# Kernel tuning notes

Measured on AMD Instinct MI355X. Metric: run time of the kernel, lower is better.

Reference implementation:

```python
import jax, jax.numpy as jnp
import numpy as np

TEMPERATURE = 0.07
NEG_INF_FILL = -1e9  # matches torch fill_diagonal_(-1000000000.0)


def setup_inputs() -> dict:
    key = jax.random.key(0)
    feats = jax.random.normal(key, (6144, 768), dtype=jnp.float32)
    return {"feats": feats}


def reference(feats):
    # L2-normalize rows (torch F.normalize uses eps=1e-12 clamp on the norm)
    norm = jnp.maximum(jnp.linalg.norm(feats, axis=1, keepdims=True), 1e-12)
    f = feats / norm
    N = f.shape[0]
    sim = jnp.matmul(f, f.T) / TEMPERATURE            # [N, N]
    eye = jnp.eye(N, dtype=bool)
    sim = jnp.where(eye, NEG_INF_FILL, sim)           # fill diagonal
    labels = jnp.arange(N) // 3                       # 3 views per slice
    pos = (labels[:, None] == labels[None, :]) & ~eye  # positives, self excluded
    # masked logsumexp over positives via weights b (grad-safe masking)
    numerator = jax.scipy.special.logsumexp(sim, axis=1, b=pos.astype(sim.dtype))
    denominator = jax.scipy.special.logsumexp(sim, axis=1)
    loss = jnp.sum(-(numerator - denominator)) / N
    return loss
```

## Files before the change

### kernel.cpp

```cpp
#include <hip/hip_runtime.h>

#define NN 6144
#define DD 768
#define NB 48
#define NTILES 1176
#define INV_T 14.285714285714286f
#define CMAX  14.285714285714286f

typedef int i32x4 __attribute__((ext_vector_type(4)));
typedef int i32x8 __attribute__((ext_vector_type(8)));
typedef float f32x4_t __attribute__((ext_vector_type(4)));

__device__ __forceinline__ void load_lds16(const void* g, void* l) {
    __builtin_amdgcn_global_load_lds((__attribute__((address_space(1))) void*)g,
                                     (__attribute__((address_space(3))) void*)l,
                                     16, 0, 0);
}

__global__ void norm_kernel(const float* __restrict__ feats,
                            unsigned int* __restrict__ fb8,
                            float* __restrict__ den_num) {
    const int wid = threadIdx.x >> 6;
    const int lane = threadIdx.x & 63;
    const int row = blockIdx.x * 4 + wid;

    if (threadIdx.x < 8) den_num[blockIdx.x * 8 + threadIdx.x] = 0.0f;

    const float4* src = (const float4*)(feats + (size_t)row * DD);
    float4 v[3];
    float ss = 0.0f;
#pragma unroll
    for (int i = 0; i < 3; ++i) {
        v[i] = src[lane + i * 64];
        ss += v[i].x * v[i].x + v[i].y * v[i].y + v[i].z * v[i].z + v[i].w * v[i].w;
    }
#pragma unroll
    for (int m = 32; m >= 1; m >>= 1) ss += __shfl_xor(ss, m);
    const float sc = 1.0f / fmaxf(sqrtf(ss), 1e-12f);

#pragma unroll
    for (int i = 0; i < 3; ++i) {
        unsigned int w = 0;
        w = __builtin_amdgcn_cvt_pk_fp8_f32(v[i].x * sc, v[i].y * sc, w, 0);
        w = __builtin_amdgcn_cvt_pk_fp8_f32(v[i].z * sc, v[i].w * sc, w, 1);
        fb8[(size_t)row * 192 + lane + i * 64] = w;
    }
}

__global__ __launch_bounds__(256, 2) void gemm_expsum_kernel(
        const unsigned char* __restrict__ fb8,
        float* __restrict__ den_sum, float* __restrict__ num_sum) {
    __shared__ __align__(16) char sA[128 * 128];
    __shared__ __align__(16) char sB[128 * 128];

    int rem = blockIdx.x;
    int bi = 0, rowlen = NB;
    while (rem >= rowlen) { rem -= rowlen; rowlen--; bi++; }
    const int bj = bi + rem;
    const bool isdiag = (bi == bj);
    const bool neardiag = (bj - bi) <= 1;
    const int i0 = bi * 128;
    const int j0 = bj * 128;

    const int t = threadIdx.x;
    const int lane = t & 63;
    const int wid = t >> 6;
    const int wm = wid >> 1;
    const int wn = wid & 1;

    const int srow = t >> 3;
    const int scb = ((t & 7) ^ (srow & 7)) * 16;
    const unsigned char* gA = fb8 + (size_t)(i0 + srow) * DD + scb;
    const unsigned char* gB = fb8 + (size_t)(j0 + srow) * DD + scb;
    char* ldsA = sA + wid * 1024;
    char* ldsB = sB + wid * 1024;

    f32x4_t acc[4][4];
    const f32x4_t zz = {0.0f, 0.0f, 0.0f, 0.0f};
#pragma unroll
    for (int mi = 0; mi < 4; ++mi)
#pragma unroll
        for (int ni = 0; ni < 4; ++ni) acc[mi][ni] = zz;

    const int q = lane >> 4;
    const int mrow = lane & 15;
    const int x7 = lane & 7;
    const int c0 = ((q << 1) ^ x7) << 4;
    const int c1 = (((q << 1) | 1) ^ x7) << 4;

#pragma unroll 1
    for (int kb = 0; kb < 6; ++kb) {
        const int k0 = kb * 128;
#pragma unroll
        for (int i = 0; i < 4; ++i) {
            load_lds16(gA + (size_t)(i * 32) * DD + k0, ldsA + i * 4096);
            load_lds16(gB + (size_t)(i * 32) * DD + k0, ldsB + i * 4096);
        }
        __syncthreads();

        i32x8 af[4];
#pragma unroll
        for (int mi = 0; mi < 4; ++mi) {
            const char* p = sA + (wm * 64 + mi * 16 + mrow) * 128;
            i32x4 lo = *(const i32x4*)(p + c0);
            i32x4 hi = *(const i32x4*)(p + c1);
            af[mi] = __builtin_shufflevector(lo, hi, 0, 1, 2, 3, 4, 5, 6, 7);
        }
#pragma unroll
        for (int ni = 0; ni < 4; ++ni) {
            const char* p = sB + (wn * 64 + ni * 16 + mrow) * 128;
            i32x4 lo = *(const i32x4*)(p + c0);
            i32x4 hi = *(const i32x4*)(p + c1);
            i32x8 bf = __builtin_shufflevector(lo, hi, 0, 1, 2, 3, 4, 5, 6, 7);
#pragma unroll
            for (int mi = 0; mi < 4; ++mi)
                acc[mi][ni] = __builtin_amdgcn_mfma_scale_f32_16x16x128_f8f6f4(
                    af[mi], bf, acc[mi][ni], 0, 0,
                    0, 0x7F7F7F7F, 0, 0x7F7F7F7F);
        }
        __syncthreads();
    }

    const int colb = j0 + wn * 64 + mrow;
    const int rowb = i0 + wm * 64 + (q << 2);
    float cs[4] = {0.f, 0.f, 0.f, 0.f};
    float csn[4] = {0.f, 0.f, 0.f, 0.f};
#pragma unroll
    for (int mi = 0; mi < 4; ++mi) {
        float rsv[4] = {0.f, 0.f, 0.f, 0.f};
        float rsn[4] = {0.f, 0.f, 0.f, 0.f};
#pragma unroll
        for (int ni = 0; ni < 4; ++ni) {
            const int col = colb + ni * 16;
#pragma unroll
            for (int r = 0; r < 4; ++r) {
                const int row = rowb + mi * 16 + r;
                const float v = acc[mi][ni][r] * INV_T;
                float e = __expf(v - CMAX);
                if (isdiag && row == col) e = 0.0f;
                rsv[r] += e;
                cs[ni] += e;
                if (neardiag && (row / 3 == col / 3) && row != col) {
                    rsn[r] += e;
                    csn[ni] += e;
                }
            }
        }
#pragma unroll
        for (int r = 0; r < 4; ++r) {
            float v = rsv[r];
            v += __shfl_xor(v, 8);
            v += __shfl_xor(v, 4);
            v += __shfl_xor(v, 2);
            v += __shfl_xor(v, 1);
            if (mrow == 0) atomicAdd(&den_sum[rowb + mi * 16 + r], v);
        }
        if (neardiag) {
#pragma unroll
            for (int r = 0; r < 4; ++r) {
                float v = rsn[r];
                v += __shfl_xor(v, 8);
                v += __shfl_xor(v, 4);
                v += __shfl_xor(v, 2);
                v += __shfl_xor(v, 1);
                if (mrow == 0) atomicAdd(&num_sum[rowb + mi * 16 + r], v);
            }
        }
    }
    if (!isdiag) {
#pragma unroll
        for (int ni = 0; ni < 4; ++ni) {
            float v = cs[ni];
            v += __shfl_xor(v, 16);
            v += __shfl_xor(v, 32);
            if (q == 0) atomicAdd(&den_sum[colb + ni * 16], v);
        }
        if (neardiag) {
#pragma unroll
            for (int ni = 0; ni < 4; ++ni) {
                float v = csn[ni];
                v += __shfl_xor(v, 16);
                v += __shfl_xor(v, 32);
                if (q == 0) atomicAdd(&num_sum[colb + ni * 16], v);
            }
        }
    }
}

__global__ void finalize_kernel(const float* __restrict__ den_sum,
                                const float* __restrict__ num_sum,
                                float* __restrict__ out) {
    float local = 0.0f;
    for (int i = threadIdx.x; i < NN; i += 256) {
        local += logf(den_sum[i]) - logf(num_sum[i]);
    }
#pragma unroll
    for (int m = 32; m >= 1; m >>= 1) local += __shfl_xor(local, m);
    __shared__ float ws[4];
    if ((threadIdx.x & 63) == 0) ws[threadIdx.x >> 6] = local;
    __syncthreads();
    if (threadIdx.x == 0) out[0] = (ws[0] + ws[1] + ws[2] + ws[3]) / (float)NN;
}

extern "C" void kernel_launch(void* const* d_in, const int* in_sizes, int n_in,
                              void* d_out, int out_size, void* d_ws, size_t ws_size,
                              hipStream_t stream) {
    const float* feats = (const float*)d_in[0];
    float* out = (float*)d_out;

    char* ws = (char*)d_ws;
    unsigned int* fb8 = (unsigned int*)ws;
    float* den_num    = (float*)(ws + 4718592);
    float* den_sum    = den_num;
    float* num_sum    = den_num + NN;

    norm_kernel<<<NN / 4, 256, 0, stream>>>(feats, fb8, den_num);
    gemm_expsum_kernel<<<NTILES, 256, 0, stream>>>((const unsigned char*)fb8,
                                                   den_sum, num_sum);
    finalize_kernel<<<1, 256, 0, stream>>>(den_sum, num_sum, out);
}
```

Before: 110.7 us.

## Double-buffer LDS tiles to overlap global loads with MFMA compute

Splits the A/B LDS tiles into two buffers each and fully unrolls the six K-steps so the next tile's global-to-LDS loads are issued before the current tile's MFMAs run. Only one barrier per step remains instead of two. It also folds the temperature scale and max shift into a single fma before exp. LDS use doubles to 64 KB per block, which may cut how many blocks fit per CU under the two-block launch bound.

New measurement: 195.4 us. +76.6%, slower.

```diff
diff --git a/kernel.cpp b/kernel.cpp
--- a/kernel.cpp
+++ b/kernel.cpp
@@ -50,8 +50,10 @@
 __global__ __launch_bounds__(256, 2) void gemm_expsum_kernel(
         const unsigned char* __restrict__ fb8,
         float* __restrict__ den_sum, float* __restrict__ num_sum) {
-    __shared__ __align__(16) char sA[128 * 128];
-    __shared__ __align__(16) char sB[128 * 128];
+    __shared__ __align__(16) char sA0[128 * 128];
+    __shared__ __align__(16) char sA1[128 * 128];
+    __shared__ __align__(16) char sB0[128 * 128];
+    __shared__ __align__(16) char sB1[128 * 128];
 
     int rem = blockIdx.x;
     int bi = 0, rowlen = NB;
@@ -72,8 +74,7 @@
     const int scb = ((t & 7) ^ (srow & 7)) * 16;
     const unsigned char* gA = fb8 + (size_t)(i0 + srow) * DD + scb;
     const unsigned char* gB = fb8 + (size_t)(j0 + srow) * DD + scb;
-    char* ldsA = sA + wid * 1024;
-    char* ldsB = sB + wid * 1024;
+    const int ldsoff = wid * 1024;
 
     f32x4_t acc[4][4];
     const f32x4_t zz = {0.0f, 0.0f, 0.0f, 0.0f};
@@ -88,38 +89,50 @@
     const int c0 = ((q << 1) ^ x7) << 4;
     const int c1 = (((q << 1) | 1) ^ x7) << 4;
 
-#pragma unroll 1
-    for (int kb = 0; kb < 6; ++kb) {
-        const int k0 = kb * 128;
-#pragma unroll
-        for (int i = 0; i < 4; ++i) {
-            load_lds16(gA + (size_t)(i * 32) * DD + k0, ldsA + i * 4096);
-            load_lds16(gB + (size_t)(i * 32) * DD + k0, ldsB + i * 4096);
-        }
-        __syncthreads();
-
-        i32x8 af[4];
-#pragma unroll
-        for (int mi = 0; mi < 4; ++mi) {
-            const char* p = sA + (wm * 64 + mi * 16 + mrow) * 128;
-            i32x4 lo = *(const i32x4*)(p + c0);
-            i32x4 hi = *(const i32x4*)(p + c1);
-            af[mi] = __builtin_shufflevector(lo, hi, 0, 1, 2, 3, 4, 5, 6, 7);
-        }
-#pragma unroll
-        for (int ni = 0; ni < 4; ++ni) {
-            const char* p = sB + (wn * 64 + ni * 16 + mrow) * 128;
-            i32x4 lo = *(const i32x4*)(p + c0);
-            i32x4 hi = *(const i32x4*)(p + c1);
-            i32x8 bf = __builtin_shufflevector(lo, hi, 0, 1, 2, 3, 4, 5, 6, 7);
-#pragma unroll
-            for (int mi = 0; mi < 4; ++mi)
-                acc[mi][ni] = __builtin_amdgcn_mfma_scale_f32_16x16x128_f8f6f4(
-                    af[mi], bf, acc[mi][ni], 0, 0,
-                    0, 0x7F7F7F7F, 0, 0x7F7F7F7F);
-        }
-        __syncthreads();
-    }
+#define STAGE(dstA, dstB, k0)                                                 \
+    {                                                                         \
+        _Pragma("unroll")                                                     \
+        for (int i = 0; i < 4; ++i) {                                         \
+            load_lds16(gA + (size_t)(i * 32) * DD + (k0), (dstA) + ldsoff + i * 4096); \
+            load_lds16(gB + (size_t)(i * 32) * DD + (k0), (dstB) + ldsoff + i * 4096); \
+        }                                                                     \
+    }
+
+#define COMPUTE(srcA, srcB)                                                   \
+    {                                                                         \
+        i32x8 af[4];                                                          \
+        _Pragma("unroll")                                                     \
+        for (int mi = 0; mi < 4; ++mi) {                                      \
+            const char* p = (srcA) + (wm * 64 + mi * 16 + mrow) * 128;        \
+            i32x4 lo = *(const i32x4*)(p + c0);                               \
+            i32x4 hi = *(const i32x4*)(p + c1);                               \
+            af[mi] = __builtin_shufflevector(lo, hi, 0, 1, 2, 3, 4, 5, 6, 7); \
+        }                                                                     \
+        _Pragma("unroll")                                                     \
+        for (int ni = 0; ni < 4; ++ni) {                                      \
+            const char* p = (srcB) + (wn * 64 + ni * 16 + mrow) * 128;        \
+            i32x4 lo = *(const i32x4*)(p + c0);                               \
+            i32x4 hi = *(const i32x4*)(p + c1);                               \
+            i32x8 bf = __builtin_shufflevector(lo, hi, 0, 1, 2, 3, 4, 5, 6, 7); \
+            _Pragma("unroll")                                                 \
+            for (int mi = 0; mi < 4; ++mi)                                    \
+                acc[mi][ni] = __builtin_amdgcn_mfma_scale_f32_16x16x128_f8f6f4( \
+                    af[mi], bf, acc[mi][ni], 0, 0,                            \
+                    0, 0x7F7F7F7F, 0, 0x7F7F7F7F);                            \
+        }                                                                     \
+    }
+
+    STAGE(sA0, sB0, 0);
+    __syncthreads();
+    STAGE(sA1, sB1, 128);  COMPUTE(sA0, sB0);  __syncthreads();
+    STAGE(sA0, sB0, 256);  COMPUTE(sA1, sB1);  __syncthreads();
+    STAGE(sA1, sB1, 384);  COMPUTE(sA0, sB0);  __syncthreads();
+    STAGE(sA0, sB0, 512);  COMPUTE(sA1, sB1);  __syncthreads();
+    STAGE(sA1, sB1, 640);  COMPUTE(sA0, sB0);  __syncthreads();
+    COMPUTE(sA1, sB1);
+
+#undef STAGE
+#undef COMPUTE
 
     const int colb = j0 + wn * 64 + mrow;
     const int rowb = i0 + wm * 64 + (q << 2);
@@ -135,8 +148,7 @@
 #pragma unroll
             for (int r = 0; r < 4; ++r) {
                 const int row = rowb + mi * 16 + r;
-                const float v = acc[mi][ni][r] * INV_T;
-                float e = __expf(v - CMAX);
+                float e = __expf(__builtin_fmaf(acc[mi][ni][r], INV_T, -CMAX));
                 if (isdiag && row == col) e = 0.0f;
                 rsv[r] += e;
                 cs[ni] += e;
```

## Switch to per-wave 64x64 tiles with direct global loads and 32x32 MFMA

Applied to the files above, without the earlier changes.

Replaces the 128x128 LDS-staged block tile with independent per-wave 64x64 upper-triangle tiles, loaded straight from global memory into registers with no LDS and no barriers. Tiles are grouped into 24x24 super-blocks and split into 8 chunks for locality, and the 16x16x128 MFMA is swapped for 32x32x64 MFMA. The goal is to remove LDS and sync overhead and raise occupancy, at the cost of less data reuse per wave (more global/L2 traffic) and more atomics per output row.

Measured after the change: 162.8 us. 1.47x slower.

```diff
diff --git a/kernel.cpp b/kernel.cpp
--- a/kernel.cpp
+++ b/kernel.cpp
@@ -2,19 +2,19 @@
 
 #define NN 6144
 #define DD 768
-#define NB 48
-#define NTILES 1176
 #define INV_T 14.285714285714286f
 #define CMAX  14.285714285714286f
 
+#define NWT 582
+
 typedef int i32x4 __attribute__((ext_vector_type(4)));
 typedef int i32x8 __attribute__((ext_vector_type(8)));
-typedef float f32x4_t __attribute__((ext_vector_type(4)));
-
-__device__ __forceinline__ void load_lds16(const void* g, void* l) {
-    __builtin_amdgcn_global_load_lds((__attribute__((address_space(1))) void*)g,
-                                     (__attribute__((address_space(3))) void*)l,
-                                     16, 0, 0);
+typedef float f32x16 __attribute__((ext_vector_type(16)));
+
+__device__ __forceinline__ i32x8 ld32B(const unsigned char* p) {
+    i32x4 lo = *(const i32x4*)p;
+    i32x4 hi = *(const i32x4*)(p + 16);
+    return __builtin_shufflevector(lo, hi, 0, 1, 2, 3, 4, 5, 6, 7);
 }
 
 __global__ void norm_kernel(const float* __restrict__ feats,
@@ -47,141 +47,120 @@
     }
 }
 
-__global__ __launch_bounds__(256, 2) void gemm_expsum_kernel(
+__global__ __launch_bounds__(256, 3) void gemm_expsum_kernel(
         const unsigned char* __restrict__ fb8,
         float* __restrict__ den_sum, float* __restrict__ num_sum) {
-    __shared__ __align__(16) char sA[128 * 128];
-    __shared__ __align__(16) char sB[128 * 128];
-
-    int rem = blockIdx.x;
-    int bi = 0, rowlen = NB;
-    while (rem >= rowlen) { rem -= rowlen; rowlen--; bi++; }
-    const int bj = bi + rem;
-    const bool isdiag = (bi == bj);
-    const bool neardiag = (bj - bi) <= 1;
-    const int i0 = bi * 128;
-    const int j0 = bj * 128;
-
-    const int t = threadIdx.x;
-    const int lane = t & 63;
-    const int wid = t >> 6;
-    const int wm = wid >> 1;
-    const int wn = wid & 1;
-
-    const int srow = t >> 3;
-    const int scb = ((t & 7) ^ (srow & 7)) * 16;
-    const unsigned char* gA = fb8 + (size_t)(i0 + srow) * DD + scb;
-    const unsigned char* gB = fb8 + (size_t)(j0 + srow) * DD + scb;
-    char* ldsA = sA + wid * 1024;
-    char* ldsB = sB + wid * 1024;
-
-    f32x4_t acc[4][4];
-    const f32x4_t zz = {0.0f, 0.0f, 0.0f, 0.0f};
-#pragma unroll
-    for (int mi = 0; mi < 4; ++mi)
-#pragma unroll
-        for (int ni = 0; ni < 4; ++ni) acc[mi][ni] = zz;
-
-    const int q = lane >> 4;
-    const int mrow = lane & 15;
-    const int x7 = lane & 7;
-    const int c0 = ((q << 1) ^ x7) << 4;
-    const int c1 = (((q << 1) | 1) ^ x7) << 4;
+    const int wid = threadIdx.x >> 6;
+    const int lane = threadIdx.x & 63;
+
+    const int chunk = blockIdx.x & 7;
+    const int pos = blockIdx.x >> 3;
+    const int qq = pos * 4 + wid;
+    if (qq >= NWT) return;
+    int rem = chunk * NWT + qq;
+
+    int si = 0;
+    while (rem >= 2028 - 576 * si) { rem -= 2028 - 576 * si; ++si; }
+    int ti, tj;
+    if (rem < 300) {
+        int r = 0;
+        while (rem >= 24 - r) { rem -= 24 - r; ++r; }
+        ti = si * 24 + r;
+        tj = si * 24 + r + rem;
+    } else {
+        rem -= 300;
+        const int sj = si + 1 + rem / 576;
+        const int lo = rem % 576;
+        ti = si * 24 + lo / 24;
+        tj = sj * 24 + lo % 24;
+    }
+    const bool isdiag = (ti == tj);
+    const bool neardiag = (tj - ti) <= 1;
+    const int i0 = ti * 64;
+    const int j0 = tj * 64;
+
+    const int l31 = lane & 31;
+    const int hi = lane >> 5;
+
+    const unsigned char* pa0 = fb8 + (size_t)(i0 + l31) * DD + hi * 32;
+    const unsigned char* pa1 = pa0 + (size_t)32 * DD;
+    const unsigned char* pb0 = fb8 + (size_t)(j0 + l31) * DD + hi * 32;
+    const unsigned char* pb1 = pb0 + (size_t)32 * DD;
+
+    f32x16 acc[2][2];
+    const f32x16 z16 = {0.f,0.f,0.f,0.f,0.f,0.f,0.f,0.f,
+                        0.f,0.f,0.f,0.f,0.f,0.f,0.f,0.f};
+    acc[0][0] = z16; acc[0][1] = z16; acc[1][0] = z16; acc[1][1] = z16;
 
 #pragma unroll 1
-    for (int kb = 0; kb < 6; ++kb) {
-        const int k0 = kb * 128;
-#pragma unroll
-        for (int i = 0; i < 4; ++i) {
-            load_lds16(gA + (size_t)(i * 32) * DD + k0, ldsA + i * 4096);
-            load_lds16(gB + (size_t)(i * 32) * DD + k0, ldsB + i * 4096);
-        }
-        __syncthreads();
-
-        i32x8 af[4];
-#pragma unroll
-        for (int mi = 0; mi < 4; ++mi) {
-            const char* p = sA + (wm * 64 + mi * 16 + mrow) * 128;
-            i32x4 lo = *(const i32x4*)(p + c0);
-            i32x4 hi = *(const i32x4*)(p + c1);
-            af[mi] = __builtin_shufflevector(lo, hi, 0, 1, 2, 3, 4, 5, 6, 7);
-        }
-#pragma unroll
-        for (int ni = 0; ni < 4; ++ni) {
-            const char* p = sB + (wn * 64 + ni * 16 + mrow) * 128;
-            i32x4 lo = *(const i32x4*)(p + c0);
-            i32x4 hi = *(const i32x4*)(p + c1);
-            i32x8 bf = __builtin_shufflevector(lo, hi, 0, 1, 2, 3, 4, 5, 6, 7);
-#pragma unroll
-            for (int mi = 0; mi < 4; ++mi)
-                acc[mi][ni] = __builtin_amdgcn_mfma_scale_f32_16x16x128_f8f6f4(
-                    af[mi], bf, acc[mi][ni], 0, 0,
-                    0, 0x7F7F7F7F, 0, 0x7F7F7F7F);
-        }
-        __syncthreads();
-    }
-
-    const int colb = j0 + wn * 64 + mrow;
-    const int rowb = i0 + wm * 64 + (q << 2);
-    float cs[4] = {0.f, 0.f, 0.f, 0.f};
-    float csn[4] = {0.f, 0.f, 0.f, 0.f};
-#pragma unroll
-    for (int mi = 0; mi < 4; ++mi) {
-        float rsv[4] = {0.f, 0.f, 0.f, 0.f};
-        float rsn[4] = {0.f, 0.f, 0.f, 0.f};
-#pragma unroll
-        for (int ni = 0; ni < 4; ++ni) {
-            const int col = colb + ni * 16;
-#pragma unroll
-            for (int r = 0; r < 4; ++r) {
-                const int row = rowb + mi * 16 + r;
-                const float v = acc[mi][ni][r] * INV_T;
-                float e = __expf(v - CMAX);
-                if (isdiag && row == col) e = 0.0f;
-                rsv[r] += e;
-                cs[ni] += e;
-                if (neardiag && (row / 3 == col / 3) && row != col) {
-                    rsn[r] += e;
-                    csn[ni] += e;
-                }
+    for (int s = 0; s < 12; ++s) {
+        const int k0 = s * 64;
+        i32x8 a0 = ld32B(pa0 + k0);
+        i32x8 a1 = ld32B(pa1 + k0);
+        i32x8 b0 = ld32B(pb0 + k0);
+        i32x8 b1 = ld32B(pb1 + k0);
+        acc[0][0] = __builtin_amdgcn_mfma_scale_f32_32x32x64_f8f6f4(
+            a0, b0, acc[0][0], 0, 0, 0, 0x7F7F7F7F, 0, 0x7F7F7F7F);
+        acc[0][1] = __builtin_amdgcn_mfma_scale_f32_32x32x64_f8f6f4(
+            a0, b1, acc[0][1], 0, 0, 0, 0x7F7F7F7F, 0, 0x7F7F7F7F);
+        acc[1][0] = __builtin_amdgcn_mfma_scale_f32_32x32x64_f8f6f4(
+            a1, b0, acc[1][0], 0, 0, 0, 0x7F7F7F7F, 0, 0x7F7F7F7F);
+        acc[1][1] = __builtin_amdgcn_mfma_scale_f32_32x32x64_f8f6f4(
+            a1, b1, acc[1][1], 0, 0, 0, 0x7F7F7F7F, 0, 0x7F7F7F7F);
+    }
+
+    float colp0 = 0.f, colp1 = 0.f, coln0 = 0.f, coln1 = 0.f;
+#pragma unroll
+    for (int mi = 0; mi < 2; ++mi) {
+#pragma unroll
+        for (int reg = 0; reg < 16; ++reg) {
+            const int row = i0 + mi * 32 + (reg & 3) + 8 * (reg >> 2) + 4 * hi;
+            const int c0 = j0 + l31;
+            const int c1 = j0 + 32 + l31;
+            float e0 = __expf(__builtin_fmaf(acc[mi][0][reg], INV_T, -CMAX));
+            float e1 = __expf(__builtin_fmaf(acc[mi][1][reg], INV_T, -CMAX));
+            if (isdiag && row == c0) e0 = 0.0f;
+            if (isdiag && row == c1) e1 = 0.0f;
+
+            float rv = e0 + e1;
+            rv += __shfl_xor(rv, 16);
+            rv += __shfl_xor(rv, 8);
+            rv += __shfl_xor(rv, 4);
+            rv += __shfl_xor(rv, 2);
+            rv += __shfl_xor(rv, 1);
+            if (l31 == 0) atomicAdd(&den_sum[row], rv);
+
+            colp0 += e0;
+            colp1 += e1;
+
+            if (neardiag) {
+                float n0 = (row != c0 && (row / 3) == (c0 / 3)) ? e0 : 0.0f;
+                float n1 = (row != c1 && (row / 3) == (c1 / 3)) ? e1 : 0.0f;
+                float rn = n0 + n1;
+                rn += __shfl_xor(rn, 16);
+                rn += __shfl_xor(rn, 8);
+                rn += __shfl_xor(rn, 4);
+                rn += __shfl_xor(rn, 2);
+                rn += __shfl_xor(rn, 1);
+                if (l31 == 0) atomicAdd(&num_sum[row], rn);
+                coln0 += n0;
+                coln1 += n1;
             }
         }
-#pragma unroll
-        for (int r = 0; r < 4; ++r) {
-            float v = rsv[r];
-            v += __shfl_xor(v, 8);
-            v += __shfl_xor(v, 4);
-            v += __shfl_xor(v, 2);
-            v += __shfl_xor(v, 1);
-            if (mrow == 0) atomicAdd(&den_sum[rowb + mi * 16 + r], v);
+    }
+    if (!isdiag) {
+        colp0 += __shfl_xor(colp0, 32);
+        colp1 += __shfl_xor(colp1, 32);
+        if (hi == 0) {
+            atomicAdd(&den_sum[j0 + l31], colp0);
+            atomicAdd(&den_sum[j0 + 32 + l31], colp1);
         }
         if (neardiag) {
-#pragma unroll
-            for (int r = 0; r < 4; ++r) {
-                float v = rsn[r];
-                v += __shfl_xor(v, 8);
-                v += __shfl_xor(v, 4);
-                v += __shfl_xor(v, 2);
-                v += __shfl_xor(v, 1);
-                if (mrow == 0) atomicAdd(&num_sum[rowb + mi * 16 + r], v);
-            }
-        }
-    }
-    if (!isdiag) {
-#pragma unroll
-        for (int ni = 0; ni < 4; ++ni) {
-            float v = cs[ni];
-            v += __shfl_xor(v, 16);
-            v += __shfl_xor(v, 32);
-            if (q == 0) atomicAdd(&den_sum[colb + ni * 16], v);
-        }
-        if (neardiag) {
-#pragma unroll
-            for (int ni = 0; ni < 4; ++ni) {
-                float v = csn[ni];
-                v += __shfl_xor(v, 16);
-                v += __shfl_xor(v, 32);
-                if (q == 0) atomicAdd(&num_sum[colb + ni * 16], v);
+            coln0 += __shfl_xor(coln0, 32);
+            coln1 += __shfl_xor(coln1, 32);
+            if (hi == 0) {
+                atomicAdd(&num_sum[j0 + l31], coln0);
+                atomicAdd(&num_sum[j0 + 32 + l31], coln1);
             }
         }
     }
@@ -215,7 +194,7 @@
     float* num_sum    = den_num + NN;
 
     norm_kernel<<<NN / 4, 256, 0, stream>>>(feats, fb8, den_num);
-    gemm_expsum_kernel<<<NTILES, 256, 0, stream>>>((const unsigned char*)fb8,
-                                                   den_sum, num_sum);
+    gemm_expsum_kernel<<<8 * 146, 256, 0, stream>>>((const unsigned char*)fb8,
+                                                    den_sum, num_sum);
     finalize_kernel<<<1, 256, 0, stream>>>(den_sum, num_sum, out);
 }
```
